# Performance work log

Measured on AMD Instinct MI355X. Metric: run time of the kernel, lower is better.

## Reference

```python
import jax, jax.numpy as jnp
import numpy as np

B, T, D, H, L, DFF, MAXLEN = 4, 2048, 512, 8, 6, 2048, 2048
DK = D // H
SCALE = float(1.0 / np.sqrt(DK * 2))  # 1/sqrt(d_k*2)


def layer_norm(x, g, b, eps=1e-5):
    m = jnp.mean(x, axis=-1, keepdims=True)
    v = jnp.var(x, axis=-1, keepdims=True)
    return (x - m) / jnp.sqrt(v + eps) * g + b


def setup_inputs() -> dict:
    key = jax.random.key(0)
    it = iter(jax.random.split(key, 48))
    def n(shape, std=0.02):
        return jax.random.normal(next(it), shape, dtype=jnp.float32) * std
    inp = {}
    inp['x'] = jax.random.normal(next(it), (B, T), dtype=jnp.float32)
    inp['ip_w'] = n((1, D)); inp['ip_b'] = jnp.zeros((D,))
    inp['ip_ln_g'] = jnp.ones((D,)); inp['ip_ln_b'] = jnp.zeros((D,))
    inp['pos_embed'] = n((MAXLEN, D), 0.01)
    inp['pad_token'] = n((D,), 0.01)
    inp['Wq'] = n((L, D, D)); inp['bq'] = jnp.zeros((L, D))
    inp['Wk'] = n((L, D, D)); inp['bk'] = jnp.zeros((L, D))
    inp['Wv'] = n((L, D, D)); inp['bv'] = jnp.zeros((L, D))
    inp['Wo'] = n((L, D, D)); inp['bo'] = jnp.zeros((L, D))
    inp['ln1_g'] = jnp.ones((L, D)); inp['ln1_b'] = jnp.zeros((L, D))
    inp['ln2_g'] = jnp.ones((L, D)); inp['ln2_b'] = jnp.zeros((L, D))
    inp['W1'] = n((L, D, DFF)); inp['b1'] = jnp.zeros((L, DFF))
    inp['W2'] = n((L, DFF, D)); inp['b2'] = jnp.zeros((L, D))
    inp['gate1'] = jnp.full((L,), 0.1); inp['gate2'] = jnp.full((L,), 0.1)
    inp['fn_g'] = jnp.ones((D,)); inp['fn_b'] = jnp.zeros((D,))
    for p in ['bh', 'ah', 'ch']:
        inp[p + '_ln_g'] = jnp.ones((D,)); inp[p + '_ln_b'] = jnp.zeros((D,))
    inp['bh_w'] = n((D, 2), 0.01); inp['bh_b'] = jnp.zeros((2,))
    inp['ah_w'] = n((D, 1), 0.01); inp['ah_b'] = jnp.zeros((1,))
    inp['ch_w'] = n((D, 1), 0.01); inp['ch_b'] = jnp.zeros((1,))
    return inp


def _forward(x, ip_w, ip_b, ip_ln_g, ip_ln_b, pos_embed, pad_token,
             Wq, bq, Wk, bk, Wv, bv, Wo, bo,
             ln1_g, ln1_b, ln2_g, ln2_b, W1, b1, W2, b2, gate1, gate2,
             fn_g, fn_b, bh_ln_g, bh_ln_b, bh_w, bh_b,
             ah_ln_g, ah_ln_b, ah_w, ah_b, ch_ln_g, ch_ln_b, ch_w, ch_b):
    Bx, Tx = x.shape
    xc = jnp.clip(x, -10.0, 10.0)
    pad_mask = xc == -1.0  # [B,T]
    h = layer_norm(xc[..., None] @ ip_w + ip_b, ip_ln_g, ip_ln_b)  # [B,T,D]
    h = h + 0.1 * pos_embed[None, :Tx, :]
    h = jnp.where(pad_mask[..., None], pad_token, h)
    cmask = jnp.triu(jnp.full((Tx, Tx), -10000.0, dtype=h.dtype), k=1)  # additive causal mask
    for i in range(L):
        xn = layer_norm(h, ln1_g[i], ln1_b[i])
        def heads(w, b, xn=xn):
            return (xn @ w + b).reshape(Bx, Tx, H, DK).transpose(0, 2, 1, 3)
        q = heads(Wq[i], bq[i]); k = heads(Wk[i], bk[i]); v = heads(Wv[i], bv[i])
        q = q / jnp.maximum(jnp.linalg.norm(q, axis=-1, keepdims=True), 1e-8)
        k = k / jnp.maximum(jnp.linalg.norm(k, axis=-1, keepdims=True), 1e-8)
        scores = jnp.clip(jnp.einsum('bhtd,bhsd->bhts', q, k) * SCALE, -5.0, 5.0) + cmask
        a = jax.nn.softmax(scores / 1.5, axis=-1)
        o = jnp.einsum('bhts,bhsd->bhtd', a, v).transpose(0, 2, 1, 3).reshape(Bx, Tx, D)
        h = h + gate1[i] * ((o @ Wo[i] + bo[i]) * 0.5)
        xn2 = layer_norm(h, ln2_g[i], ln2_b[i])
        ffn = jax.nn.gelu(xn2 @ W1[i] + b1[i], approximate=False) @ W2[i] + b2[i]
        h = jnp.clip(h + gate2[i] * ffn, -10.0, 10.0)
    h = layer_norm(h, fn_g, fn_b)
    m = (~pad_mask).astype(h.dtype)[..., None]
    mean = (h * m).sum(axis=1) / jnp.maximum(m.sum(axis=1), 1.0)  # masked mean pool [B,D]
    binary = layer_norm(mean, bh_ln_g, bh_ln_b) @ bh_w + bh_b
    anomaly = layer_norm(mean, ah_ln_g, ah_ln_b) @ ah_w + ah_b
    caustic = jax.nn.sigmoid(layer_norm(mean, ch_ln_g, ch_ln_b) @ ch_w + ch_b)
    return jnp.concatenate([binary, anomaly, caustic], axis=-1)  # [B,4]


def reference(x, ip_w, ip_b, ip_ln_g, ip_ln_b, pos_embed, pad_token,
              Wq, bq, Wk, bk, Wv, bv, Wo, bo,
              ln1_g, ln1_b, ln2_g, ln2_b, W1, b1, W2, b2, gate1, gate2,
              fn_g, fn_b, bh_ln_g, bh_ln_b, bh_w, bh_b,
              ah_ln_g, ah_ln_b, ah_w, ah_b, ch_ln_g, ch_ln_b, ch_w, ch_b):
    return _forward(x, ip_w, ip_b, ip_ln_g, ip_ln_b, pos_embed, pad_token,
                    Wq, bq, Wk, bk, Wv, bv, Wo, bo,
                    ln1_g, ln1_b, ln2_g, ln2_b, W1, b1, W2, b2, gate1, gate2,
                    fn_g, fn_b, bh_ln_g, bh_ln_b, bh_w, bh_b,
                    ah_ln_g, ah_ln_b, ah_w, ah_b, ch_ln_g, ch_ln_b, ch_w, ch_b)
```

## Files before the change

### kernel.cpp

```cpp
#include <hip/hip_runtime.h>
#include <hip/hip_bf16.h>
#include <math.h>

constexpr int Bsz = 4, T = 2048, D = 512, H = 8, Lnum = 6, DFF = 2048, DK = 64;
constexpr int QS2 = 1024;
constexpr float K2 = 0.08838834764831845f / 1.5f;

typedef __attribute__((ext_vector_type(8))) short svec8;
typedef __attribute__((ext_vector_type(4))) float fvec4;

__device__ __forceinline__ fvec4 mfma16(svec8 a, svec8 b, fvec4 c) {
    return __builtin_amdgcn_mfma_f32_16x16x32_bf16(a, b, c, 0, 0, 0);
}
__device__ __forceinline__ unsigned short f2b(float f) {
    unsigned int u = __float_as_uint(f);
    u += 0x7fffu + ((u >> 16) & 1u);
    return (unsigned short)(u >> 16);
}
__device__ __forceinline__ unsigned int pk2b(float a, float b) {
    __hip_bfloat162 h = __float22bfloat162_rn(float2{a, b});
    return *(unsigned int*)&h;
}
__device__ __forceinline__ float wave_red_sum(float v) {
    for (int o = 32; o > 0; o >>= 1) v += __shfl_down(v, o, 64);
    return __shfl(v, 0, 64);
}
__device__ __forceinline__ void glds16(const unsigned short* g, unsigned short* l) {
    __builtin_amdgcn_global_load_lds(
        (const __attribute__((address_space(1))) unsigned int*)g,
        (__attribute__((address_space(3))) unsigned int*)l, 16, 0, 0);
}
#define WAITVM(n) __builtin_amdgcn_s_waitcnt(0x0F70 | ((n) & 0xF) | ((((n) >> 4) & 3) << 14))
#define FRAG(buf, row, kq) (*(const svec8*)((buf) + (((row) << 6) | ((((kq) ^ ((row) & 7))) << 3))))

__global__ __launch_bounds__(64)
void embed_kernel(const float* __restrict__ x, const float* __restrict__ ip_w,
                  const float* __restrict__ ip_b, const float* __restrict__ g,
                  const float* __restrict__ bta, const float* __restrict__ pos,
                  const float* __restrict__ pad_tok, float* __restrict__ h)
{
    int row = blockIdx.x;
    int t = row & (T - 1);
    int lane = threadIdx.x;
    float xv = x[row];
    float xc = fminf(fmaxf(xv, -10.f), 10.f);
    bool pad = (xc == -1.0f);
    float pre[8];
    float s = 0.f, s2 = 0.f;
#pragma unroll
    for (int j = 0; j < 8; j++) {
        int d = j * 64 + lane;
        float p = xc * ip_w[d] + ip_b[d];
        pre[j] = p; s += p; s2 += p * p;
    }
    s = wave_red_sum(s); s2 = wave_red_sum(s2);
    float m = s * (1.f / 512.f);
    float var = s2 * (1.f / 512.f) - m * m;
    float rstd = 1.f / sqrtf(var + 1e-5f);
#pragma unroll
    for (int j = 0; j < 8; j++) {
        int d = j * 64 + lane;
        float hv = (pre[j] - m) * rstd * g[d] + bta[d] + 0.1f * pos[(size_t)t * D + d];
        if (pad) hv = pad_tok[d];
        h[(size_t)row * D + d] = hv;
    }
}

__global__ __launch_bounds__(256)
void ln_kernel(const float* __restrict__ in, float* __restrict__ out,
               const float* __restrict__ g, const float* __restrict__ b)
{
    int row = blockIdx.x * 4 + (threadIdx.x >> 6);
    int lane = threadIdx.x & 63;
    const float* r = in + (size_t)row * D;
    float4 v0 = ((const float4*)r)[lane];
    float4 v1 = ((const float4*)r)[lane + 64];
    float s = v0.x + v0.y + v0.z + v0.w + v1.x + v1.y + v1.z + v1.w;
    float s2 = v0.x*v0.x + v0.y*v0.y + v0.z*v0.z + v0.w*v0.w
             + v1.x*v1.x + v1.y*v1.y + v1.z*v1.z + v1.w*v1.w;
    s = wave_red_sum(s); s2 = wave_red_sum(s2);
    float m = s * (1.f / 512.f);
    float var = s2 * (1.f / 512.f) - m * m;
    float rstd = 1.f / sqrtf(var + 1e-5f);
    float4 g0 = ((const float4*)g)[lane], g1 = ((const float4*)g)[lane + 64];
    float4 b0 = ((const float4*)b)[lane], b1 = ((const float4*)b)[lane + 64];
    float4 o0, o1;
    o0.x = (v0.x - m) * rstd * g0.x + b0.x; o0.y = (v0.y - m) * rstd * g0.y + b0.y;
    o0.z = (v0.z - m) * rstd * g0.z + b0.z; o0.w = (v0.w - m) * rstd * g0.w + b0.w;
    o1.x = (v1.x - m) * rstd * g1.x + b1.x; o1.y = (v1.y - m) * rstd * g1.y + b1.y;
    o1.z = (v1.z - m) * rstd * g1.z + b1.z; o1.w = (v1.w - m) * rstd * g1.w + b1.w;
    ((float4*)(out + (size_t)row * D))[lane] = o0;
    ((float4*)(out + (size_t)row * D))[lane + 64] = o1;
}

__device__ __forceinline__ void ln_row_bf16(const float* __restrict__ in, unsigned short* __restrict__ out,
                                            const float* __restrict__ g, const float* __restrict__ b,
                                            int row, int lane)
{
    const float* r = in + (size_t)row * D;
    float4 v0 = ((const float4*)r)[lane];
    float4 v1 = ((const float4*)r)[lane + 64];
    float s = v0.x + v0.y + v0.z + v0.w + v1.x + v1.y + v1.z + v1.w;
    float s2 = v0.x*v0.x + v0.y*v0.y + v0.z*v0.z + v0.w*v0.w
             + v1.x*v1.x + v1.y*v1.y + v1.z*v1.z + v1.w*v1.w;
    s = wave_red_sum(s); s2 = wave_red_sum(s2);
    float m = s * (1.f / 512.f);
    float var = s2 * (1.f / 512.f) - m * m;
    float rstd = 1.f / sqrtf(var + 1e-5f);
    float4 g0 = ((const float4*)g)[lane], g1 = ((const float4*)g)[lane + 64];
    float4 b0 = ((const float4*)b)[lane], b1 = ((const float4*)b)[lane + 64];
    unsigned short o0[4], o1[4];
    o0[0] = f2b((v0.x - m) * rstd * g0.x + b0.x); o0[1] = f2b((v0.y - m) * rstd * g0.y + b0.y);
    o0[2] = f2b((v0.z - m) * rstd * g0.z + b0.z); o0[3] = f2b((v0.w - m) * rstd * g0.w + b0.w);
    o1[0] = f2b((v1.x - m) * rstd * g1.x + b1.x); o1[1] = f2b((v1.y - m) * rstd * g1.y + b1.y);
    o1[2] = f2b((v1.z - m) * rstd * g1.z + b1.z); o1[3] = f2b((v1.w - m) * rstd * g1.w + b1.w);
    *(uint2*)(out + (size_t)row * D + lane * 4) = *(uint2*)o0;
    *(uint2*)(out + (size_t)row * D + 256 + lane * 4) = *(uint2*)o1;
}

__global__ __launch_bounds__(256)
void ln_bf16_kernel(const float* __restrict__ in, unsigned short* __restrict__ out,
                    const float* __restrict__ g, const float* __restrict__ b)
{
    ln_row_bf16(in, out, g, b, blockIdx.x * 4 + (threadIdx.x >> 6), threadIdx.x & 63);
}

__global__ __launch_bounds__(256)
void prep_kernel(const float* __restrict__ wq, const float* __restrict__ wk,
                 const float* __restrict__ wv, const float* __restrict__ wo,
                 const float* __restrict__ w1, const float* __restrict__ w2,
                 unsigned short* __restrict__ oq, unsigned short* __restrict__ ok,
                 unsigned short* __restrict__ ov, unsigned short* __restrict__ oo,
                 unsigned short* __restrict__ o1, unsigned short* __restrict__ o2,
                 const float* __restrict__ hin, unsigned short* __restrict__ lnout,
                 const float* __restrict__ ln_g, const float* __restrict__ ln_b)
{
    __shared__ float tile[32][33];
    int bid = blockIdx.x;
    if (bid >= 3072) {
        int row = (bid - 3072) * 4 + (threadIdx.x >> 6);
        ln_row_bf16(hin, lnout, ln_g, ln_b, row, threadIdx.x & 63);
        return;
    }
    const float* in; unsigned short* out; int K, N, kt, nt;
    if (bid < 1024) {
        int sel = bid >> 8, loc = bid & 255;
        in  = sel == 0 ? wq : sel == 1 ? wk : sel == 2 ? wv : wo;
        out = sel == 0 ? oq : sel == 1 ? ok : sel == 2 ? ov : oo;
        K = 512; N = 512; kt = loc >> 4; nt = loc & 15;
    } else if (bid < 2048) {
        int loc = bid - 1024; in = w1; out = o1; K = 512; N = 2048; kt = loc >> 6; nt = loc & 63;
    } else {
        int loc = bid - 2048; in = w2; out = o2; K = 2048; N = 512; kt = loc >> 4; nt = loc & 15;
    }
    int k0 = kt * 32, n0 = nt * 32;
    int t = threadIdx.x;
    int kr = t >> 3, nc = (t & 7) * 4;
    float4 v = *(const float4*)(in + (size_t)(k0 + kr) * N + n0 + nc);
    tile[kr][nc] = v.x; tile[kr][nc + 1] = v.y; tile[kr][nc + 2] = v.z; tile[kr][nc + 3] = v.w;
    __syncthreads();
    unsigned short o[4];
#pragma unroll
    for (int i = 0; i < 4; i++) o[i] = f2b(tile[nc + i][kr]);
    *(uint2*)(out + (size_t)(n0 + kr) * K + k0 + nc) = *(uint2*)o;
}

template<int EPI, int OBF, int BM>
__global__ __launch_bounds__(256)
void gemm_bf16(const unsigned short* __restrict__ A, const unsigned short* __restrict__ BT,
               const float* __restrict__ bias, const float* __restrict__ bias_b,
               const float* __restrict__ bias_c, const float* __restrict__ res,
               void* __restrict__ Cv, unsigned short* __restrict__ vtout,
               int M, int N, int K, const float* __restrict__ gate_p)
{
    constexpr int WN = (BM == 128) ? 2 : 4;
    constexpr int WSPAN = 128 / WN;
    constexpr int NT = WSPAN / 16;
    constexpr int MT = 4;
    constexpr int ACALLS = BM / 32;
    constexpr int SMEMSZ = (EPI == 0) ? 17408 : (BM * 64 + 128 * 64);
    __shared__ __align__(16) unsigned short SMEM[SMEMSZ];
    unsigned short* As = SMEM;
    unsigned short* Bs = SMEM + BM * 64;
    const int tid = threadIdx.x, w = tid >> 6, lane = tid & 63, quad = lane >> 4, ln = lane & 15;
    const int wm = w / WN, wn = w % WN;
    const int m0 = blockIdx.x * BM, n0 = blockIdx.y * 128;
    const int jg = (lane & 7) ^ ((lane >> 3) & 7);
    const int rb = w * 8 + (lane >> 3);
    const unsigned short* Agl = A + (size_t)(m0 + rb) * K + jg * 8;
    const unsigned short* Bgl = BT + (size_t)(n0 + rb) * K + jg * 8;

    fvec4 acc[MT][NT];
#pragma unroll
    for (int mt = 0; mt < MT; mt++)
#pragma unroll
        for (int nt = 0; nt < NT; nt++)
#pragma unroll
            for (int r = 0; r < 4; r++) acc[mt][nt][r] = 0.f;

    for (int k0 = 0; k0 < K; k0 += 64) {
        __syncthreads();
#pragma unroll
        for (int c = 0; c < ACALLS; c++)
            glds16(Agl + k0 + (size_t)c * 32 * K, As + c * 2048 + w * 512);
#pragma unroll
        for (int c = 0; c < 4; c++)
            glds16(Bgl + k0 + (size_t)c * 32 * K, Bs + c * 2048 + w * 512);
        __syncthreads();
#pragma unroll
        for (int kk = 0; kk < 2; kk++) {
            svec8 af[MT], bfr[NT];
#pragma unroll
            for (int mt = 0; mt < MT; mt++)
                af[mt] = FRAG(As, wm * 64 + mt * 16 + ln, kk * 4 + quad);
#pragma unroll
            for (int nt = 0; nt < NT; nt++)
                bfr[nt] = FRAG(Bs, wn * WSPAN + nt * 16 + ln, kk * 4 + quad);
#pragma unroll
            for (int mt = 0; mt < MT; mt++)
#pragma unroll
                for (int nt = 0; nt < NT; nt++)
                    acc[mt][nt] = mfma16(af[mt], bfr[nt], acc[mt][nt]);
        }
    }

    const float gate = (EPI == 1 || EPI == 3) ? gate_p[0] : 0.f;
    float bb[NT];
#pragma unroll
    for (int nt = 0; nt < NT; nt++) {
        int n = n0 + wn * WSPAN + nt * 16 + ln;
        if (EPI == 0) {
            int nseg = n >> 9;
            const float* bsel = nseg == 0 ? bias : (nseg == 1 ? bias_b : bias_c);
            bb[nt] = bsel[n - nseg * 512];
        } else {
            bb[nt] = bias[n];
        }
    }

    if (EPI == 0 && n0 >= 1024) {
        __syncthreads();
#pragma unroll
        for (int mt = 0; mt < MT; mt++) {
#pragma unroll
            for (int nt = 0; nt < NT; nt++) {
                int nl = wn * 64 + nt * 16 + ln;
                int mb = wm * 64 + mt * 16 + quad * 4;
                unsigned int lo = pk2b(acc[mt][nt][0] + bb[nt], acc[mt][nt][1] + bb[nt]);
                unsigned int hi = pk2b(acc[mt][nt][2] + bb[nt], acc[mt][nt][3] + bb[nt]);
                uint2 u; u.x = lo; u.y = hi;
                *(uint2*)(SMEM + nl * 136 + mb) = u;
            }
        }
        __syncthreads();
        int row = tid >> 1, half = (tid & 1) * 64;
        unsigned short* dst = vtout + ((size_t)((m0 >> 11) * 512 + (n0 - 1024) + row)) * T
                              + (m0 & (T - 1)) + half;
        const unsigned short* src = SMEM + row * 136 + half;
#pragma unroll
        for (int j = 0; j < 8; j++) *(uint4*)(dst + j * 8) = *(const uint4*)(src + j * 8);
        return;
    }

#pragma unroll
    for (int mt = 0; mt < MT; mt++) {
        float v[NT][4];
#pragma unroll
        for (int nt = 0; nt < NT; nt++)
#pragma unroll
            for (int r = 0; r < 4; r++) v[nt][r] = acc[mt][nt][r] + bb[nt];
        if (EPI == 0) {
            const float fac = ((n0 + wn * WSPAN) < 512) ? K2 : 1.f;
#pragma unroll
            for (int r = 0; r < 4; r++) {
                float s = 0.f;
#pragma unroll
                for (int nt = 0; nt < NT; nt++) s += v[nt][r] * v[nt][r];
                s += __shfl_xor(s, 1); s += __shfl_xor(s, 2);
                s += __shfl_xor(s, 4); s += __shfl_xor(s, 8);
                float rs = fac / fmaxf(sqrtf(s), 1e-8f);
#pragma unroll
                for (int nt = 0; nt < NT; nt++) v[nt][r] *= rs;
            }
        }
#pragma unroll
        for (int nt = 0; nt < NT; nt++) {
            int n = n0 + wn * WSPAN + nt * 16 + ln;
#pragma unroll
            for (int r = 0; r < 4; r++) {
                int m = m0 + wm * 64 + mt * 16 + quad * 4 + r;
                float val = v[nt][r];
                if (EPI == 0) {
                    ((unsigned short*)Cv)[(size_t)m * QS2 + n] = f2b(val);
                } else {
                    size_t off = (size_t)m * N + n;
                    if (EPI == 1) val = res[off] + gate * 0.5f * val;
                    else if (EPI == 2) {
                        float u = val;
                        float z = 0.7978845608028654f * fmaf(0.044715f * u, u * u, u);
                        float e = __builtin_amdgcn_exp2f(z * 2.8853900817779268f);
                        float rr = __builtin_amdgcn_rcpf(e + 1.f);
                        val = u * (1.f - rr);
                    }
                    else if (EPI == 3) val = fminf(fmaxf(res[off] + gate * val, -10.f), 10.f);
                    if (OBF) ((unsigned short*)Cv)[off] = f2b(val);
                    else ((float*)Cv)[off] = val;
                }
            }
        }
    }
}

template<bool DIAG>
__device__ __forceinline__ void attn_step64(
    unsigned short* Psw, const unsigned short* Ks, const unsigned short* Vt,
    const svec8 (&qf)[4][2], fvec4 (&oacc)[4][4], fvec4 (&lacc)[4],
    int quad, int ln)
{
    constexpr short BONE = (short)0x3F80;
    const svec8 ONES8 = {BONE, BONE, BONE, BONE, BONE, BONE, BONE, BONE};
#pragma unroll
    for (int nt = 0; nt < 4; nt++) {
        svec8 kf0 = FRAG(Ks, nt * 16 + ln, quad);
        svec8 kf1 = FRAG(Ks, nt * 16 + ln, 4 + quad);
        const int sbase = nt * 16 + quad * 4;
#pragma unroll
        for (int qg = 0; qg < 4; qg++) {
            fvec4 z; z[0] = z[1] = z[2] = z[3] = 0.f;
            z = mfma16(kf0, qf[qg][0], z);
            z = mfma16(kf1, qf[qg][1], z);
            const int qcol = qg * 16 + ln;
            float p[4];
#pragma unroll
            for (int r = 0; r < 4; r++) {
                float y = z[r];
                float pv = fmaf(y, fmaf(y, 0.5f, 1.f), 1.f);
                if (DIAG && (sbase + r > qcol)) pv = 0.f;
                p[r] = pv;
            }
            uint2 u; u.x = pk2b(p[0], p[1]); u.y = pk2b(p[2], p[3]);
            const int paddr = (qcol << 6) | ((((sbase >> 3) ^ (qcol & 7))) << 3) | (sbase & 7);
            *(uint2*)(Psw + paddr) = u;
        }
    }
#pragma unroll
    for (int ks = 0; ks < 2; ks++) {
        svec8 pa[4];
#pragma unroll
        for (int qm = 0; qm < 4; qm++) {
            pa[qm] = FRAG(Psw, qm * 16 + ln, ks * 4 + quad);
            lacc[qm] = mfma16(pa[qm], ONES8, lacc[qm]);
        }
#pragma unroll
        for (int dkn = 0; dkn < 4; dkn++) {
            svec8 vf = FRAG(Vt, dkn * 16 + ln, ks * 4 + quad);
#pragma unroll
            for (int qm = 0; qm < 4; qm++)
                oacc[qm][dkn] = mfma16(pa[qm], vf, oacc[qm][dkn]);
        }
    }
}

__global__ __launch_bounds__(128)
void attn_kernel(const unsigned short* __restrict__ qkv, const unsigned short* __restrict__ vt,
                 unsigned short* __restrict__ o)
{
    __shared__ __align__(16) unsigned short Kb[2][2][4096];
    __shared__ __align__(16) unsigned short Vb[2][2][4096];
    __shared__ __align__(16) unsigned short Ps[2][4096];
    const int fid = blockIdx.x;
    const int c = fid & 255, slot = fid >> 8, k = c >> 5;
    const int bh = c & 31;
    const int qt = (slot == 0) ? k : (slot == 1) ? 15 - k : (slot == 2) ? 16 + k : 31 - k;
    const int b = bh >> 3, hh = bh & 7;
    const int nst = qt + 1;
    const int tid = threadIdx.x, w = tid >> 6, lane = tid & 63, quad = lane >> 4, ln = lane & 15;
    const int jgz = (lane & 7) ^ (lane >> 3);

    svec8 qf[4][2];
#pragma unroll
    for (int qg = 0; qg < 4; qg++) {
        const unsigned short* qp = qkv + ((size_t)(b * T + qt * 64 + qg * 16 + ln)) * QS2 + hh * 64;
        qf[qg][0] = *(const svec8*)(qp + quad * 8);
        qf[qg][1] = *(const svec8*)(qp + 32 + quad * 8);
    }

    const unsigned short* kbase = qkv + ((size_t)(b * T) + (lane >> 3)) * QS2 + 512 + hh * 64 + jgz * 8;
    const unsigned short* vbase = vt + ((size_t)(bh * 64) + (lane >> 3)) * T + jgz * 8;

    fvec4 oacc[4][4], lacc[4];
#pragma unroll
    for (int qm = 0; qm < 4; qm++) {
#pragma unroll
        for (int r = 0; r < 4; r++) lacc[qm][r] = 0.f;
#pragma unroll
        for (int dkn = 0; dkn < 4; dkn++)
#pragma unroll
            for (int r = 0; r < 4; r++) oacc[qm][dkn][r] = 0.f;
    }

    if (w < nst) {
#pragma unroll
        for (int cc = 0; cc < 8; cc++) {
            glds16(kbase + ((size_t)(w * 64) + cc * 8) * QS2, Kb[w][0] + cc * 512);
            glds16(vbase + (size_t)(cc * 8) * T + w * 64, Vb[w][0] + cc * 512);
        }
        int buf = 0;
        for (int s = w; s < nst; s += 2, buf ^= 1) {
            const int snext = s + 2;
            const bool pre = (snext < nst);
            if (pre) {
#pragma unroll
                for (int cc = 0; cc < 8; cc++) {
                    glds16(kbase + ((size_t)(snext * 64) + cc * 8) * QS2, Kb[w][buf ^ 1] + cc * 512);
                    glds16(vbase + (size_t)(cc * 8) * T + snext * 64, Vb[w][buf ^ 1] + cc * 512);
                }
                WAITVM(16);
            } else {
                WAITVM(0);
            }
            __builtin_amdgcn_sched_barrier(0);
            if (s == qt) attn_step64<true >(Ps[w], Kb[w][buf], Vb[w][buf], qf, oacc, lacc, quad, ln);
            else         attn_step64<false>(Ps[w], Kb[w][buf], Vb[w][buf], qf, oacc, lacc, quad, ln);
        }
    }

    __syncthreads();
    float* red = (float*)&Kb[0][0][0];
    float* mine = red + w * 5120 + lane * 80;
#pragma unroll
    for (int qm = 0; qm < 4; qm++) {
#pragma unroll
        for (int dkn = 0; dkn < 4; dkn++)
#pragma unroll
            for (int r = 0; r < 4; r++) mine[qm * 16 + dkn * 4 + r] = oacc[qm][dkn][r];
#pragma unroll
        for (int r = 0; r < 4; r++) mine[64 + qm * 4 + r] = lacc[qm][r];
    }
    __syncthreads();
    const float* other = red + (w ^ 1) * 5120 + lane * 80;
#pragma unroll
    for (int half = 0; half < 2; half++) {
        const int qm = w * 2 + half;
        float lsum[4];
#pragma unroll
        for (int r = 0; r < 4; r++) lsum[r] = lacc[qm][r] + other[64 + qm * 4 + r];
        unsigned short* og = o + (size_t)(b * T + qt * 64 + qm * 16 + quad * 4) * D + hh * 64;
#pragma unroll
        for (int r = 0; r < 4; r++) {
            float inv = 1.f / lsum[r];
#pragma unroll
            for (int dkn = 0; dkn < 4; dkn++) {
                float osum = oacc[qm][dkn][r] + other[qm * 16 + dkn * 4 + r];
                og[(size_t)r * D + dkn * 16 + ln] = f2b(osum * inv);
            }
        }
    }
}

__global__ __launch_bounds__(256)
void pool_kernel(const float* __restrict__ hn, const float* __restrict__ x, float* __restrict__ part)
{
    int b = blockIdx.x, ch = blockIdx.y, tid = threadIdx.x;
    int t0 = ch * 128;
    float s0 = 0.f, s1 = 0.f, cnt = 0.f;
    for (int tt = 0; tt < 128; tt++) {
        int t = t0 + tt;
        float xv = x[b * T + t];
        float m = (xv == -1.0f) ? 0.f : 1.f;
        cnt += m;
        const float* r = hn + ((size_t)(b * T + t)) * D;
        s0 += r[tid] * m;
        s1 += r[tid + 256] * m;
    }
    float* pr = part + (size_t)(b * 16 + ch) * 513;
    pr[tid] = s0; pr[tid + 256] = s1;
    if (tid == 0) pr[512] = cnt;
}

__global__ __launch_bounds__(64)
void head_kernel(const float* __restrict__ part,
                 const float* __restrict__ bh_g, const float* __restrict__ bh_bl,
                 const float* __restrict__ ah_g, const float* __restrict__ ah_bl,
                 const float* __restrict__ ch_g, const float* __restrict__ ch_bl,
                 const float* __restrict__ bh_w, const float* __restrict__ bh_b2,
                 const float* __restrict__ ah_w, const float* __restrict__ ah_b2,
                 const float* __restrict__ ch_w, const float* __restrict__ ch_b2,
                 float* __restrict__ out)
{
    int b = blockIdx.x, lane = threadIdx.x;
    float cnt = 0.f;
    for (int c = 0; c < 16; c++) cnt += part[(size_t)(b * 16 + c) * 513 + 512];
    float denom = fmaxf(cnt, 1.f);
    float md[8];
    float s = 0.f, s2 = 0.f;
#pragma unroll
    for (int j = 0; j < 8; j++) {
        int d = j * 64 + lane;
        float acc = 0.f;
        for (int c = 0; c < 16; c++) acc += part[(size_t)(b * 16 + c) * 513 + d];
        md[j] = acc / denom;
        s += md[j]; s2 += md[j] * md[j];
    }
    s = wave_red_sum(s); s2 = wave_red_sum(s2);
    float mu = s * (1.f / 512.f);
    float var = s2 * (1.f / 512.f) - mu * mu;
    float rstd = 1.f / sqrtf(var + 1e-5f);
    float a0 = 0.f, a1 = 0.f, a2 = 0.f, a3 = 0.f;
#pragma unroll
    for (int j = 0; j < 8; j++) {
        int d = j * 64 + lane;
        float z = (md[j] - mu) * rstd;
        float zb = z * bh_g[d] + bh_bl[d];
        a0 += zb * bh_w[d * 2 + 0];
        a1 += zb * bh_w[d * 2 + 1];
        a2 += (z * ah_g[d] + ah_bl[d]) * ah_w[d];
        a3 += (z * ch_g[d] + ch_bl[d]) * ch_w[d];
    }
    a0 = wave_red_sum(a0); a1 = wave_red_sum(a1);
    a2 = wave_red_sum(a2); a3 = wave_red_sum(a3);
    if (lane == 0) {
        out[b * 4 + 0] = a0 + bh_b2[0];
        out[b * 4 + 1] = a1 + bh_b2[1];
        out[b * 4 + 2] = a2 + ah_b2[0];
        float t3 = a3 + ch_b2[0];
        out[b * 4 + 3] = 1.f / (1.f + expf(-t3));
    }
}

extern "C" void kernel_launch(void* const* d_in, const int* in_sizes, int n_in,
                              void* d_out, int out_size, void* d_ws, size_t ws_size,
                              hipStream_t stream)
{
    const float* x      = (const float*)d_in[0];
    const float* ip_w   = (const float*)d_in[1];
    const float* ip_b   = (const float*)d_in[2];
    const float* ip_ln_g= (const float*)d_in[3];
    const float* ip_ln_b= (const float*)d_in[4];
    const float* pos    = (const float*)d_in[5];
    const float* pad_tok= (const float*)d_in[6];
    const float* Wq = (const float*)d_in[7];  const float* bq = (const float*)d_in[8];
    const float* Wk = (const float*)d_in[9];  const float* bk = (const float*)d_in[10];
    const float* Wv = (const float*)d_in[11]; const float* bv = (const float*)d_in[12];
    const float* Wo = (const float*)d_in[13]; const float* bo = (const float*)d_in[14];
    const float* ln1_g = (const float*)d_in[15]; const float* ln1_b = (const float*)d_in[16];
    const float* ln2_g = (const float*)d_in[17]; const float* ln2_b = (const float*)d_in[18];
    const float* W1 = (const float*)d_in[19]; const float* b1 = (const float*)d_in[20];
    const float* W2 = (const float*)d_in[21]; const float* b2 = (const float*)d_in[22];
    const float* gate1 = (const float*)d_in[23]; const float* gate2 = (const float*)d_in[24];
    const float* fn_g = (const float*)d_in[25]; const float* fn_b = (const float*)d_in[26];
    const float* bh_g  = (const float*)d_in[27]; const float* bh_bl = (const float*)d_in[28];
    const float* ah_g  = (const float*)d_in[29]; const float* ah_bl = (const float*)d_in[30];
    const float* ch_g  = (const float*)d_in[31]; const float* ch_bl = (const float*)d_in[32];
    const float* bh_w  = (const float*)d_in[33]; const float* bh_b2 = (const float*)d_in[34];
    const float* ah_w  = (const float*)d_in[35]; const float* ah_b2 = (const float*)d_in[36];
    const float* ch_w  = (const float*)d_in[37]; const float* ch_b2 = (const float*)d_in[38];

    char* ws = (char*)d_ws;
    float*          h     = (float*)ws;
    unsigned short* act_b = (unsigned short*)(ws + 16777216);
    unsigned short* qkv   = (unsigned short*)(ws + 25165824);
    unsigned short* mid_b = (unsigned short*)(ws + 41943040);
    float*          xn_f  = (float*)(ws + 41943040);
    unsigned short* wT    = (unsigned short*)(ws + 75497472);
    unsigned short* vt    = (unsigned short*)(ws + 81788928);
    float*          part  = (float*)(ws + 90177536);
    float*          out   = (float*)d_out;

    unsigned short* wqT = wT;
    unsigned short* wkT = wT + 262144;
    unsigned short* wvT = wT + 524288;
    unsigned short* woT = wT + 786432;
    unsigned short* w1T = wT + 1048576;
    unsigned short* w2T = wT + 2097152;

    embed_kernel<<<dim3(Bsz * T), dim3(64), 0, stream>>>(x, ip_w, ip_b, ip_ln_g, ip_ln_b, pos, pad_tok, h);

    for (int i = 0; i < Lnum; i++) {
        const size_t dd = (size_t)i * D * D;
        const size_t df = (size_t)i * D * DFF;
        prep_kernel<<<dim3(5120), dim3(256), 0, stream>>>(Wq + dd, Wk + dd, Wv + dd, Wo + dd,
                                                          W1 + df, W2 + df,
                                                          wqT, wkT, wvT, woT, w1T, w2T,
                                                          h, act_b, ln1_g + i * D, ln1_b + i * D);
        gemm_bf16<0, 1, 128><<<dim3(64, 12), dim3(256), 0, stream>>>(act_b, wqT, bq + i * D, bk + i * D, bv + i * D,
                                                                     nullptr, qkv, vt, Bsz * T, 1536, D, nullptr);
        attn_kernel<<<dim3(1024), dim3(128), 0, stream>>>(qkv, vt, act_b);
        gemm_bf16<1, 0, 64><<<dim3(128, 4), dim3(256), 0, stream>>>(act_b, woT, bo + i * D, nullptr, nullptr,
                                                                    h, h, nullptr, Bsz * T, D, D, gate1 + i);
        ln_bf16_kernel<<<dim3(Bsz * T / 4), dim3(256), 0, stream>>>(h, act_b, ln2_g + i * D, ln2_b + i * D);
        gemm_bf16<2, 1, 128><<<dim3(64, 16), dim3(256), 0, stream>>>(act_b, w1T, b1 + i * DFF, nullptr, nullptr,
                                                                     nullptr, mid_b, nullptr, Bsz * T, DFF, D, nullptr);
        gemm_bf16<3, 0, 64><<<dim3(128, 4), dim3(256), 0, stream>>>(mid_b, w2T, b2 + i * D, nullptr, nullptr,
                                                                    h, h, nullptr, Bsz * T, D, DFF, gate2 + i);
    }

    ln_kernel<<<dim3(Bsz * T / 4), dim3(256), 0, stream>>>(h, xn_f, fn_g, fn_b);
    pool_kernel<<<dim3(Bsz, 16), dim3(256), 0, stream>>>(xn_f, x, part);
    head_kernel<<<dim3(Bsz), dim3(64), 0, stream>>>(part, bh_g, bh_bl, ah_g, ah_bl, ch_g, ch_bl,
                                                    bh_w, bh_b2, ah_w, ah_b2, ch_w, ch_b2, out);
}
```

Measured before the change: 1.315 ms.

## Split attention block by query rows instead of key tiles across waves

Each of the two waves now owns 32 query rows and walks all key tiles. Before, each wave owned all 64 query rows and half of the key tiles, with an LDS reduction of partial outputs at the end. K/V tiles are loaded cooperatively into shared LDS, two tiles per phase with block-wide barriers. This removes the cross-wave reduction and halves per-wave accumulator registers. In exchange, the per-wave asynchronous double-buffer prefetch is replaced by synchronous load-then-compute phases, so load latency is no longer overlapped with compute.

```diff
diff --git a/kernel.cpp b/kernel.cpp
--- a/kernel.cpp
+++ b/kernel.cpp
@@ -30,7 +30,6 @@
         (const __attribute__((address_space(1))) unsigned int*)g,
         (__attribute__((address_space(3))) unsigned int*)l, 16, 0, 0);
 }
-#define WAITVM(n) __builtin_amdgcn_s_waitcnt(0x0F70 | ((n) & 0xF) | ((((n) >> 4) & 3) << 14))
 #define FRAG(buf, row, kq) (*(const svec8*)((buf) + (((row) << 6) | ((((kq) ^ ((row) & 7))) << 3))))
 
 __global__ __launch_bounds__(64)
@@ -312,10 +311,10 @@
 }
 
 template<bool DIAG>
-__device__ __forceinline__ void attn_step64(
-    unsigned short* Psw, const unsigned short* Ks, const unsigned short* Vt,
-    const svec8 (&qf)[4][2], fvec4 (&oacc)[4][4], fvec4 (&lacc)[4],
-    int quad, int ln)
+__device__ __forceinline__ void attn_step32(
+    unsigned short* Ps, const unsigned short* Ks, const unsigned short* Vt,
+    const svec8 (&qf)[2][2], fvec4 (&oacc)[2][4], fvec4 (&lacc)[2],
+    int w, int quad, int ln)
 {
     constexpr short BONE = (short)0x3F80;
     const svec8 ONES8 = {BONE, BONE, BONE, BONE, BONE, BONE, BONE, BONE};
@@ -325,11 +324,11 @@
         svec8 kf1 = FRAG(Ks, nt * 16 + ln, 4 + quad);
         const int sbase = nt * 16 + quad * 4;
 #pragma unroll
-        for (int qg = 0; qg < 4; qg++) {
+        for (int qg = 0; qg < 2; qg++) {
             fvec4 z; z[0] = z[1] = z[2] = z[3] = 0.f;
             z = mfma16(kf0, qf[qg][0], z);
             z = mfma16(kf1, qf[qg][1], z);
-            const int qcol = qg * 16 + ln;
+            const int qcol = w * 32 + qg * 16 + ln;
             float p[4];
 #pragma unroll
             for (int r = 0; r < 4; r++) {
@@ -340,23 +339,23 @@
             }
             uint2 u; u.x = pk2b(p[0], p[1]); u.y = pk2b(p[2], p[3]);
             const int paddr = (qcol << 6) | ((((sbase >> 3) ^ (qcol & 7))) << 3) | (sbase & 7);
-            *(uint2*)(Psw + paddr) = u;
+            *(uint2*)(Ps + paddr) = u;
         }
     }
 #pragma unroll
     for (int ks = 0; ks < 2; ks++) {
-        svec8 pa[4];
-#pragma unroll
-        for (int qm = 0; qm < 4; qm++) {
-            pa[qm] = FRAG(Psw, qm * 16 + ln, ks * 4 + quad);
-            lacc[qm] = mfma16(pa[qm], ONES8, lacc[qm]);
+        svec8 pa[2];
+#pragma unroll
+        for (int qg = 0; qg < 2; qg++) {
+            pa[qg] = FRAG(Ps, w * 32 + qg * 16 + ln, ks * 4 + quad);
+            lacc[qg] = mfma16(pa[qg], ONES8, lacc[qg]);
         }
 #pragma unroll
         for (int dkn = 0; dkn < 4; dkn++) {
             svec8 vf = FRAG(Vt, dkn * 16 + ln, ks * 4 + quad);
 #pragma unroll
-            for (int qm = 0; qm < 4; qm++)
-                oacc[qm][dkn] = mfma16(pa[qm], vf, oacc[qm][dkn]);
+            for (int qg = 0; qg < 2; qg++)
+                oacc[qg][dkn] = mfma16(pa[qg], vf, oacc[qg][dkn]);
         }
     }
 }
@@ -365,9 +364,8 @@
 void attn_kernel(const unsigned short* __restrict__ qkv, const unsigned short* __restrict__ vt,
                  unsigned short* __restrict__ o)
 {
-    __shared__ __align__(16) unsigned short Kb[2][2][4096];
-    __shared__ __align__(16) unsigned short Vb[2][2][4096];
-    __shared__ __align__(16) unsigned short Ps[2][4096];
+    __shared__ __align__(16) unsigned short K0[4096], V0[4096], K1[4096], V1[4096];
+    __shared__ __align__(16) unsigned short Ps[4096];
     const int fid = blockIdx.x;
     const int c = fid & 255, slot = fid >> 8, k = c >> 5;
     const int bh = c & 31;
@@ -377,83 +375,63 @@
     const int tid = threadIdx.x, w = tid >> 6, lane = tid & 63, quad = lane >> 4, ln = lane & 15;
     const int jgz = (lane & 7) ^ (lane >> 3);
 
-    svec8 qf[4][2];
-#pragma unroll
-    for (int qg = 0; qg < 4; qg++) {
-        const unsigned short* qp = qkv + ((size_t)(b * T + qt * 64 + qg * 16 + ln)) * QS2 + hh * 64;
+    svec8 qf[2][2];
+#pragma unroll
+    for (int qg = 0; qg < 2; qg++) {
+        const unsigned short* qp = qkv + ((size_t)(b * T + qt * 64 + w * 32 + qg * 16 + ln)) * QS2 + hh * 64;
         qf[qg][0] = *(const svec8*)(qp + quad * 8);
         qf[qg][1] = *(const svec8*)(qp + 32 + quad * 8);
     }
 
-    const unsigned short* kbase = qkv + ((size_t)(b * T) + (lane >> 3)) * QS2 + 512 + hh * 64 + jgz * 8;
-    const unsigned short* vbase = vt + ((size_t)(bh * 64) + (lane >> 3)) * T + jgz * 8;
-
-    fvec4 oacc[4][4], lacc[4];
-#pragma unroll
-    for (int qm = 0; qm < 4; qm++) {
-#pragma unroll
-        for (int r = 0; r < 4; r++) lacc[qm][r] = 0.f;
+    const unsigned short* kbase = qkv + ((size_t)(b * T) + w * 8 + (lane >> 3)) * QS2 + 512 + hh * 64 + jgz * 8;
+    const unsigned short* vbase = vt + ((size_t)(bh * 64) + w * 8 + (lane >> 3)) * T + jgz * 8;
+    const int ldsoff = w * 8 * 64;
+
+    fvec4 oacc[2][4], lacc[2];
+#pragma unroll
+    for (int qg = 0; qg < 2; qg++) {
+#pragma unroll
+        for (int r = 0; r < 4; r++) lacc[qg][r] = 0.f;
 #pragma unroll
         for (int dkn = 0; dkn < 4; dkn++)
 #pragma unroll
-            for (int r = 0; r < 4; r++) oacc[qm][dkn][r] = 0.f;
-    }
-
-    if (w < nst) {
-#pragma unroll
-        for (int cc = 0; cc < 8; cc++) {
-            glds16(kbase + ((size_t)(w * 64) + cc * 8) * QS2, Kb[w][0] + cc * 512);
-            glds16(vbase + (size_t)(cc * 8) * T + w * 64, Vb[w][0] + cc * 512);
-        }
-        int buf = 0;
-        for (int s = w; s < nst; s += 2, buf ^= 1) {
-            const int snext = s + 2;
-            const bool pre = (snext < nst);
-            if (pre) {
-#pragma unroll
-                for (int cc = 0; cc < 8; cc++) {
-                    glds16(kbase + ((size_t)(snext * 64) + cc * 8) * QS2, Kb[w][buf ^ 1] + cc * 512);
-                    glds16(vbase + (size_t)(cc * 8) * T + snext * 64, Vb[w][buf ^ 1] + cc * 512);
-                }
-                WAITVM(16);
-            } else {
-                WAITVM(0);
+            for (int r = 0; r < 4; r++) oacc[qg][dkn][r] = 0.f;
+    }
+
+    const int Nph = (nst + 1) >> 1;
+    for (int ph = 0; ph < Nph; ph++) {
+        const int s0 = 2 * ph, s1 = 2 * ph + 1;
+        __syncthreads();
+#pragma unroll
+        for (int cc = 0; cc < 4; cc++) {
+            glds16(kbase + ((size_t)(s0 * 64) + cc * 16) * QS2, K0 + cc * 1024 + ldsoff);
+            glds16(vbase + (size_t)(cc * 16) * T + s0 * 64, V0 + cc * 1024 + ldsoff);
+        }
+        if (s1 < nst) {
+#pragma unroll
+            for (int cc = 0; cc < 4; cc++) {
+                glds16(kbase + ((size_t)(s1 * 64) + cc * 16) * QS2, K1 + cc * 1024 + ldsoff);
+                glds16(vbase + (size_t)(cc * 16) * T + s1 * 64, V1 + cc * 1024 + ldsoff);
             }
-            __builtin_amdgcn_sched_barrier(0);
-            if (s == qt) attn_step64<true >(Ps[w], Kb[w][buf], Vb[w][buf], qf, oacc, lacc, quad, ln);
-            else         attn_step64<false>(Ps[w], Kb[w][buf], Vb[w][buf], qf, oacc, lacc, quad, ln);
-        }
-    }
-
-    __syncthreads();
-    float* red = (float*)&Kb[0][0][0];
-    float* mine = red + w * 5120 + lane * 80;
-#pragma unroll
-    for (int qm = 0; qm < 4; qm++) {
-#pragma unroll
-        for (int dkn = 0; dkn < 4; dkn++)
-#pragma unroll
-            for (int r = 0; r < 4; r++) mine[qm * 16 + dkn * 4 + r] = oacc[qm][dkn][r];
-#pragma unroll
-        for (int r = 0; r < 4; r++) mine[64 + qm * 4 + r] = lacc[qm][r];
-    }
-    __syncthreads();
-    const float* other = red + (w ^ 1) * 5120 + lane * 80;
-#pragma unroll
-    for (int half = 0; half < 2; half++) {
-        const int qm = w * 2 + half;
-        float lsum[4];
-#pragma unroll
-        for (int r = 0; r < 4; r++) lsum[r] = lacc[qm][r] + other[64 + qm * 4 + r];
-        unsigned short* og = o + (size_t)(b * T + qt * 64 + qm * 16 + quad * 4) * D + hh * 64;
+        }
+        __syncthreads();
+        if (s0 == qt) attn_step32<true >(Ps, K0, V0, qf, oacc, lacc, w, quad, ln);
+        else          attn_step32<false>(Ps, K0, V0, qf, oacc, lacc, w, quad, ln);
+        if (s1 < nst) {
+            if (s1 == qt) attn_step32<true >(Ps, K1, V1, qf, oacc, lacc, w, quad, ln);
+            else          attn_step32<false>(Ps, K1, V1, qf, oacc, lacc, w, quad, ln);
+        }
+    }
+
+    unsigned short* og = o + (size_t)(b * T + qt * 64 + w * 32 + quad * 4) * D + hh * 64;
+#pragma unroll
+    for (int qg = 0; qg < 2; qg++) {
 #pragma unroll
         for (int r = 0; r < 4; r++) {
-            float inv = 1.f / lsum[r];
-#pragma unroll
-            for (int dkn = 0; dkn < 4; dkn++) {
-                float osum = oacc[qm][dkn][r] + other[qm * 16 + dkn * 4 + r];
-                og[(size_t)r * D + dkn * 16 + ln] = f2b(osum * inv);
-            }
+            float inv = 1.f / lacc[qg][r];
+#pragma unroll
+            for (int dkn = 0; dkn < 4; dkn++)
+                og[(size_t)(qg * 16 + r) * D + dkn * 16 + ln] = f2b(oacc[qg][dkn][r] * inv);
         }
     }
 }
```

Result: faster. 1.182 ms (-10.1%).
